# Kernel optimization log

Measured on AMD Instinct MI355X. Metric: run time of the kernel, lower is better.

Reference implementation:

```python
import jax, jax.numpy as jnp
import numpy as np

D_MODEL = 1024
N_HEAD = 16
DPH = D_MODEL // N_HEAD
NEG = -1e18


def setup_inputs() -> dict:
    key = jax.random.key(0)
    ks = jax.random.split(key, 8)
    B, L = 4, 2048
    k = jax.random.normal(ks[0], (B, L, D_MODEL), dtype=jnp.float32)
    v = jax.random.normal(ks[1], (B, L, D_MODEL), dtype=jnp.float32)
    q = jax.random.normal(ks[2], (B, L, D_MODEL), dtype=jnp.float32)
    attn_mask = jax.random.randint(ks[3], (B, L, L), 0, 2, dtype=jnp.int32)
    query_mask = jnp.ones((B, L), dtype=jnp.float32)
    # xavier_uniform bounds
    bnd1 = float(np.sqrt(6.0 / (3 * D_MODEL + D_MODEL)))
    bnd2 = float(np.sqrt(6.0 / (2 * D_MODEL)))
    kqv_w = jax.random.uniform(ks[4], (3 * D_MODEL, D_MODEL), minval=-bnd1, maxval=bnd1, dtype=jnp.float32)
    kqv_b = jnp.zeros((3 * D_MODEL,), dtype=jnp.float32)
    fin_w = jax.random.uniform(ks[5], (D_MODEL, D_MODEL), minval=-bnd2, maxval=bnd2, dtype=jnp.float32)
    fin_b = jnp.zeros((D_MODEL,), dtype=jnp.float32)
    return {"k": k, "v": v, "q": q, "attn_mask": attn_mask, "query_mask": query_mask,
            "kqv_w": kqv_w, "kqv_b": kqv_b, "fin_w": fin_w, "fin_b": fin_b}


def _split_heads(x, B):
    # [B, L, D] -> [B, H, L, dph]
    return x.reshape(B, -1, N_HEAD, DPH).transpose(0, 2, 1, 3)


def reference(k, v, q, attn_mask, query_mask, kqv_w, kqv_b, fin_w, fin_b):
    B = k.shape[0]
    scaling = DPH ** (-0.5)
    # three separate projections from one fused weight tensor (as in original)
    kp = k @ kqv_w[0:D_MODEL, :].T + kqv_b[0:D_MODEL]
    qp = q @ kqv_w[D_MODEL:2 * D_MODEL, :].T + kqv_b[D_MODEL:2 * D_MODEL]
    vp = v @ kqv_w[2 * D_MODEL:, :].T + kqv_b[2 * D_MODEL:]
    kh = _split_heads(kp, B)
    qh = _split_heads(qp, B) * scaling
    vh = _split_heads(vp, B)
    attn = jnp.einsum('bhqd,bhkd->bhqk', qh, kh)  # [B,H,Lq,Lk]
    if attn_mask is not None:
        attn = jnp.where(attn_mask[:, None, :, :] != 0, NEG, attn)
    attn = jax.nn.softmax(attn, axis=-1)
    # dropout: identity (eval mode / deterministic reference)
    context = jnp.einsum('bhqk,bhkd->bhqd', attn, vh)
    context = context.transpose(0, 2, 1, 3).reshape(B, -1, D_MODEL)
    context = context @ fin_w.T + fin_b
    attn_avg = attn.sum(axis=1) / N_HEAD  # [B,Lq,Lk]
    if query_mask is not None:
        qm = query_mask[:, :, None]
        context = context * qm
        attn_avg = attn_avg * qm
    return (context, attn_avg)
```

## Files before the change

kernel.cpp:

```cpp
#include <hip/hip_runtime.h>
#include <stdint.h>


typedef unsigned short u16;
typedef __attribute__((ext_vector_type(8))) short short8;
typedef __attribute__((ext_vector_type(4))) float f32x4;
typedef __attribute__((ext_vector_type(4))) float float4v;
typedef __attribute__((ext_vector_type(2))) unsigned int uint2v;

__device__ __forceinline__ u16 f2bf(float f){
  union { float f; uint32_t i; } c; c.f = f;
  return (u16)((c.i + 0x7FFFu + ((c.i >> 16) & 1u)) >> 16);
}
__device__ __forceinline__ short8 ld8(const u16* p){ return *(const short8*)p; }
__device__ __forceinline__ short8 ld8f(const float* p){
  const float4v a = *(const float4v*)p;
  const float4v b = *(const float4v*)(p + 4);
  short8 r;
  r[0] = (short)f2bf(a[0]); r[1] = (short)f2bf(a[1]);
  r[2] = (short)f2bf(a[2]); r[3] = (short)f2bf(a[3]);
  r[4] = (short)f2bf(b[0]); r[5] = (short)f2bf(b[1]);
  r[6] = (short)f2bf(b[2]); r[7] = (short)f2bf(b[3]);
  return r;
}
__device__ __forceinline__ float exp2_fast(float x){
  float r; asm("v_exp_f32 %0, %1" : "=v"(r) : "v"(x)); return r;
}
__device__ __forceinline__ uint32_t cvt_pk_bf16(float lo, float hi){
  uint32_t r;
  asm("v_cvt_pk_bf16_f32 %0, %1, %2" : "=v"(r) : "v"(lo), "v"(hi));
  return r;
}

#define MFMA(a,b,c) __builtin_amdgcn_mfma_f32_16x16x32_bf16((a),(b),(c),0,0,0)

__global__ void sentinel_k(float* out, float v){ out[0] = v; }

__global__ __launch_bounds__(256) void maskpack_k(const int* __restrict__ m,
                                                  uint64_t* __restrict__ bits){
  int t = blockIdx.x * 256 + threadIdx.x;
  uint64_t b = __ballot(m[t] != 0);
  if ((threadIdx.x & 63) == 0) bits[t >> 6] = b;
}

#define QLDA 40
__global__ __launch_bounds__(256) void qkv_gemm_k(
    const float* __restrict__ kin, const float* __restrict__ qin, const float* __restrict__ vin,
    const float* __restrict__ w, const float* __restrict__ bias,
    u16* __restrict__ qh, u16* __restrict__ kh, u16* __restrict__ vt)
{
  const int z = blockIdx.z;
  const float* A = (z == 0) ? kin : (z == 1) ? qin : vin;
  const float* W = w + (size_t)z * 1024 * 1024;
  const float* bs = bias + z * 1024;
  const int tileM = blockIdx.y * 64, tileN = blockIdx.x * 64;
  __shared__ __align__(16) u16 As[64 * QLDA];
  __shared__ __align__(16) u16 Bs[64 * QLDA];
  const int t = threadIdx.x, wave = t >> 6, lane = t & 63, quad = lane >> 4, mm = lane & 15;
  const int waveM = (wave >> 1) * 32, waveN = (wave & 1) * 32;
  f32x4 acc[2][2];
  for (int i = 0; i < 2; i++) for (int j = 0; j < 2; j++) acc[i][j] = (f32x4){0.f,0.f,0.f,0.f};
  const int lr = t >> 2, lc = (t & 3) * 8;
  for (int k0 = 0; k0 < 1024; k0 += 32){
    __syncthreads();
    *(short8*)&As[lr * QLDA + lc] = ld8f(&A[(size_t)(tileM + lr) * 1024 + k0 + lc]);
    *(short8*)&Bs[lr * QLDA + lc] = ld8f(&W[(size_t)(tileN + lr) * 1024 + k0 + lc]);
    __syncthreads();
    short8 a0 = *(const short8*)&As[(waveM + mm) * QLDA + quad * 8];
    short8 a1 = *(const short8*)&As[(waveM + 16 + mm) * QLDA + quad * 8];
    short8 b0 = *(const short8*)&Bs[(waveN + mm) * QLDA + quad * 8];
    short8 b1 = *(const short8*)&Bs[(waveN + 16 + mm) * QLDA + quad * 8];
    acc[0][0] = MFMA(a0, b0, acc[0][0]);
    acc[0][1] = MFMA(a0, b1, acc[0][1]);
    acc[1][0] = MFMA(a1, b0, acc[1][0]);
    acc[1][1] = MFMA(a1, b1, acc[1][1]);
  }
  const float scale = (z == 1) ? 0.18033688011112042f : 1.0f;
  for (int i = 0; i < 2; i++) for (int j = 0; j < 2; j++){
    int col = tileN + waveN + j * 16 + mm;
    float bv = bs[col];
    int h = col >> 6, d = col & 63;
    for (int r = 0; r < 4; r++){
      int row = tileM + waveM + i * 16 + quad * 4 + r;
      int bb = row >> 11, l = row & 2047;
      float v = (acc[i][j][r] + bv) * scale;
      if (z == 2)      vt[((bb * 16 + h) * 64 + d) * 2048 + l] = f2bf(v);
      else if (z == 1) qh[((bb * 16 + h) * 2048 + l) * 64 + d] = f2bf(v);
      else             kh[((bb * 16 + h) * 2048 + l) * 64 + d] = f2bf(v);
    }
  }
}

#define LDK 72
#define LDV 136
__global__ __launch_bounds__(256, 4) void flash_k(
    const u16* __restrict__ qh, const u16* __restrict__ kh, const u16* __restrict__ vt,
    const uint64_t* __restrict__ maskbits, u16* __restrict__ ctx,
    float* __restrict__ statsM, float* __restrict__ statsL)
{
  const int b = blockIdx.z, h = blockIdx.y, q0 = blockIdx.x * 64;
  const int t = threadIdx.x, wave = t >> 6, lane = t & 63, quad = lane >> 4, mm = lane & 15;
  __shared__ __align__(16) u16 Ks[128 * LDK];
  __shared__ __align__(16) u16 Vs[64 * LDV];
  const u16* qb = qh + (size_t)((b * 16 + h) * 2048) * 64;
  const u16* kb = kh + (size_t)((b * 16 + h) * 2048) * 64;
  const u16* vb = vt + (size_t)((b * 16 + h) * 64) * 2048;
  const int qrow = q0 + wave * 16 + mm;
  short8 qa0 = ld8(&qb[qrow * 64 + quad * 8]);
  short8 qa1 = ld8(&qb[qrow * 64 + 32 + quad * 8]);
  f32x4 O[4];
  for (int cb = 0; cb < 4; cb++) O[cb] = (f32x4){0.f,0.f,0.f,0.f};
  float mr = -30000.0f, lrn = 0.f;
  const uint64_t* mrow = maskbits + (size_t)(b * 2048 + qrow) * 32;

  for (int kt = 0; kt < 16; kt++){
    const int k0 = kt * 128;
    __syncthreads();
    #pragma unroll
    for (int i = 0; i < 4; i++){
      int ch = t + i * 256;
      int row = ch >> 3, c8 = (ch & 7) * 8;
      *(short8*)&Ks[row * LDK + c8] = ld8(&kb[(k0 + row) * 64 + c8]);
    }
    #pragma unroll
    for (int i = 0; i < 4; i++){
      int ch = t + i * 256;
      int row = ch >> 4, c8 = (ch & 15) * 8;
      *(short8*)&Vs[row * LDV + c8] = ld8(&vb[row * 2048 + k0 + c8]);
    }
    __syncthreads();
    f32x4 S[8];
    #pragma unroll
    for (int cb = 0; cb < 8; cb++){
      S[cb] = (f32x4){0.f,0.f,0.f,0.f};
      short8 kb0 = *(const short8*)&Ks[(cb * 16 + mm) * LDK + quad * 8];
      short8 kb1 = *(const short8*)&Ks[(cb * 16 + mm) * LDK + 32 + quad * 8];
      S[cb] = MFMA(kb0, qa0, S[cb]);
      S[cb] = MFMA(kb1, qa1, S[cb]);
    }
    uint64_t wq0 = mrow[2 * kt]     >> (quad * 4);
    uint64_t wq1 = mrow[2 * kt + 1] >> (quad * 4);
    #pragma unroll
    for (int cb = 0; cb < 8; cb++){
      uint32_t bits = (uint32_t)(((cb < 4) ? wq0 : wq1) >> (16 * (cb & 3)));
      #pragma unroll
      for (int r = 0; r < 4; r++)
        if (bits & (1u << r)) S[cb][r] = -1e30f;
    }
    f32x4 m4 = S[0];
    #pragma unroll
    for (int cb = 1; cb < 8; cb++)
      #pragma unroll
      for (int r = 0; r < 4; r++) m4[r] = fmaxf(m4[r], S[cb][r]);
    float tmax = fmaxf(fmaxf(m4[0], m4[1]), fmaxf(m4[2], m4[3]));
    tmax = fmaxf(tmax, __shfl_xor(tmax, 16, 64));
    tmax = fmaxf(tmax, __shfl_xor(tmax, 32, 64));
    float mnew  = fmaxf(mr, tmax);
    float alpha = exp2_fast(mr - mnew);
    f32x4 s4 = (f32x4){0.f,0.f,0.f,0.f};
    #pragma unroll
    for (int cb = 0; cb < 8; cb++)
      #pragma unroll
      for (int r = 0; r < 4; r++){
        float p = exp2_fast(S[cb][r] - mnew);
        S[cb][r] = p; s4[r] += p;
      }
    float tsum = (s4[0] + s4[1]) + (s4[2] + s4[3]);
    tsum += __shfl_xor(tsum, 16, 64);
    tsum += __shfl_xor(tsum, 32, 64);
    lrn = lrn * alpha + tsum;
    mr  = mnew;
    #pragma unroll
    for (int r = 0; r < 4; r++){
      float aq = __shfl(alpha, (lane & 48) | (quad * 4 + r), 64);
      #pragma unroll
      for (int cb = 0; cb < 4; cb++) O[cb][r] *= aq;
    }
    #pragma unroll
    for (int kc = 0; kc < 4; kc++){
      union { short8 s; uint32_t u[4]; } pa;
      pa.u[0] = cvt_pk_bf16(S[2 * kc][0],     S[2 * kc][1]);
      pa.u[1] = cvt_pk_bf16(S[2 * kc][2],     S[2 * kc][3]);
      pa.u[2] = cvt_pk_bf16(S[2 * kc + 1][0], S[2 * kc + 1][1]);
      pa.u[3] = cvt_pk_bf16(S[2 * kc + 1][2], S[2 * kc + 1][3]);
      #pragma unroll
      for (int cb = 0; cb < 4; cb++){
        union { short8 s; uint32_t u[4]; } vv;
        const uint2v vlo = *(const uint2v*)&Vs[(cb * 16 + mm) * LDV + kc * 32 + quad * 4];
        const uint2v vhi = *(const uint2v*)&Vs[(cb * 16 + mm) * LDV + kc * 32 + 16 + quad * 4];
        vv.u[0] = vlo[0]; vv.u[1] = vlo[1];
        vv.u[2] = vhi[0]; vv.u[3] = vhi[1];
        O[cb] = MFMA(pa.s, vv.s, O[cb]);
      }
    }
  }
  float inv = (lrn > 0.f) ? 1.0f / lrn : 0.f;
  #pragma unroll
  for (int r = 0; r < 4; r++){
    float invq = __shfl(inv, (lane & 48) | (quad * 4 + r), 64);
    int qg = q0 + wave * 16 + quad * 4 + r;
    #pragma unroll
    for (int cb = 0; cb < 4; cb++)
      ctx[(size_t)(b * 2048 + qg) * 1024 + h * 64 + cb * 16 + mm] = f2bf(O[cb][r] * invq);
  }
  if (quad == 0){
    statsM[(b * 16 + h) * 2048 + qrow] = mr;
    statsL[(b * 16 + h) * 2048 + qrow] = lrn;
  }
}

__global__ __launch_bounds__(256) void attnavg_k(
    const u16* __restrict__ qh, const u16* __restrict__ kh,
    const uint64_t* __restrict__ maskbits, const float* __restrict__ statsM,
    const float* __restrict__ statsL, const float* __restrict__ qmask,
    float* __restrict__ out2)
{
  const int b = blockIdx.z, q0 = blockIdx.y * 64, k0 = blockIdx.x * 64;
  const int t = threadIdx.x, wave = t >> 6, lane = t & 63, quad = lane >> 4, mm = lane & 15;
  __shared__ __align__(16) u16 Ks[64 * LDK];
  f32x4 acc[4];
  for (int cb = 0; cb < 4; cb++) acc[cb] = (f32x4){0.f,0.f,0.f,0.f};
  const int qg0 = q0 + wave * 16 + quad * 4;
  uint64_t wb[4];
  for (int r = 0; r < 4; r++)
    wb[r] = maskbits[(size_t)(b * 2048 + qg0 + r) * 32 + (k0 >> 6)];
  const int lr_ = t >> 2, lc_ = (t & 3) * 8;

  for (int h = 0; h < 16; h++){
    const u16* kb = kh + (size_t)((b * 16 + h) * 2048) * 64;
    const u16* qb = qh + (size_t)((b * 16 + h) * 2048) * 64;
    __syncthreads();
    *(short8*)&Ks[lr_ * LDK + lc_]      = ld8(&kb[(k0 + lr_) * 64 + lc_]);
    *(short8*)&Ks[lr_ * LDK + 32 + lc_] = ld8(&kb[(k0 + lr_) * 64 + 32 + lc_]);
    __syncthreads();
    const int qrow = q0 + wave * 16 + mm;
    short8 qa0 = ld8(&qb[qrow * 64 + quad * 8]);
    short8 qa1 = ld8(&qb[qrow * 64 + 32 + quad * 8]);
    f32x4 S[4];
    #pragma unroll
    for (int cb = 0; cb < 4; cb++){
      S[cb] = (f32x4){0.f,0.f,0.f,0.f};
      short8 kb0 = *(const short8*)&Ks[(cb * 16 + mm) * LDK + quad * 8];
      short8 kb1 = *(const short8*)&Ks[(cb * 16 + mm) * LDK + 32 + quad * 8];
      S[cb] = MFMA(qa0, kb0, S[cb]);
      S[cb] = MFMA(qa1, kb1, S[cb]);
    }
    #pragma unroll
    for (int r = 0; r < 4; r++){
      int sidx = (b * 16 + h) * 2048 + qg0 + r;
      float mh = statsM[sidx], lh = statsL[sidx];
      float sc = (lh > 0.f) ? 1.0f / (lh * 16.0f) : 0.f;
      #pragma unroll
      for (int cb = 0; cb < 4; cb++)
        if (!((wb[r] >> (cb * 16 + mm)) & 1ull))
          acc[cb][r] += exp2_fast(S[cb][r] - mh) * sc;
    }
  }
  for (int r = 0; r < 4; r++){
    int qg = qg0 + r;
    float qm = qmask[b * 2048 + qg];
    for (int cb = 0; cb < 4; cb++)
      out2[(size_t)(b * 2048 + qg) * 2048 + k0 + cb * 16 + mm] = acc[cb][r] * qm;
  }
}

__global__ __launch_bounds__(256) void fin_gemm_k(
    const u16* __restrict__ A, const float* __restrict__ W, const float* __restrict__ bias,
    const float* __restrict__ qmask, float* __restrict__ out)
{
  const int tileM = blockIdx.y * 64, tileN = blockIdx.x * 64;
  __shared__ __align__(16) u16 As[64 * QLDA];
  __shared__ __align__(16) u16 Bs[64 * QLDA];
  const int t = threadIdx.x, wave = t >> 6, lane = t & 63, quad = lane >> 4, mm = lane & 15;
  const int waveM = (wave >> 1) * 32, waveN = (wave & 1) * 32;
  f32x4 acc[2][2];
  for (int i = 0; i < 2; i++) for (int j = 0; j < 2; j++) acc[i][j] = (f32x4){0.f,0.f,0.f,0.f};
  const int lr = t >> 2, lc = (t & 3) * 8;
  for (int k0 = 0; k0 < 1024; k0 += 32){
    __syncthreads();
    *(short8*)&As[lr * QLDA + lc] = ld8(&A[(size_t)(tileM + lr) * 1024 + k0 + lc]);
    *(short8*)&Bs[lr * QLDA + lc] = ld8f(&W[(size_t)(tileN + lr) * 1024 + k0 + lc]);
    __syncthreads();
    short8 a0 = *(const short8*)&As[(waveM + mm) * QLDA + quad * 8];
    short8 a1 = *(const short8*)&As[(waveM + 16 + mm) * QLDA + quad * 8];
    short8 b0 = *(const short8*)&Bs[(waveN + mm) * QLDA + quad * 8];
    short8 b1 = *(const short8*)&Bs[(waveN + 16 + mm) * QLDA + quad * 8];
    acc[0][0] = MFMA(a0, b0, acc[0][0]);
    acc[0][1] = MFMA(a0, b1, acc[0][1]);
    acc[1][0] = MFMA(a1, b0, acc[1][0]);
    acc[1][1] = MFMA(a1, b1, acc[1][1]);
  }
  for (int i = 0; i < 2; i++) for (int j = 0; j < 2; j++){
    int col = tileN + waveN + j * 16 + mm;
    float bv = bias[col];
    for (int r = 0; r < 4; r++){
      int row = tileM + waveM + i * 16 + quad * 4 + r;
      float v = (acc[i][j][r] + bv) * qmask[row];
      out[(size_t)row * 1024 + col] = v;
    }
  }
}

extern "C" void kernel_launch(void* const* d_in, const int* in_sizes, int n_in,
                              void* d_out, int out_size, void* d_ws, size_t ws_size,
                              hipStream_t stream) {
  const float* k_in   = (const float*)d_in[0];
  const float* v_in   = (const float*)d_in[1];
  const float* q_in   = (const float*)d_in[2];
  const int*   amask  = (const int*)d_in[3];
  const float* qmask  = (const float*)d_in[4];
  const float* kqv_w  = (const float*)d_in[5];
  const float* kqv_b  = (const float*)d_in[6];
  const float* fin_w  = (const float*)d_in[7];
  const float* fin_b  = (const float*)d_in[8];
  float* out  = (float*)d_out;
  float* out2 = out + (size_t)8388608;

  const size_t WS_NEED = 36700160;
  if (ws_size < WS_NEED){
    sentinel_k<<<1, 1, 0, stream>>>(out, 1.0e6f + (float)(ws_size >> 20));
    return;
  }

  u16* qh  = (u16*)d_ws;
  u16* kh  = qh + (size_t)8388608;
  float* statsM = (float*)(kh + (size_t)8388608);
  float* statsL = statsM + 131072;
  uint64_t* maskbits = (uint64_t*)(statsL + 131072);
  u16* vt  = (u16*)out;
  u16* ctx = (u16*)out2;

  maskpack_k<<<dim3(65536), dim3(256), 0, stream>>>(amask, maskbits);
  qkv_gemm_k<<<dim3(16, 128, 3), dim3(256), 0, stream>>>(
      k_in, q_in, v_in, kqv_w, kqv_b, qh, kh, vt);
  flash_k<<<dim3(32, 16, 4), dim3(256), 0, stream>>>(
      qh, kh, vt, maskbits, ctx, statsM, statsL);
  fin_gemm_k<<<dim3(16, 128), dim3(256), 0, stream>>>(
      ctx, fin_w, fin_b, qmask, out);
  attnavg_k<<<dim3(32, 32, 4), dim3(256), 0, stream>>>(
      qh, kh, maskbits, statsM, statsL, qmask, out2);
}
```

Before: 771.4 us.

## Enlarge projection GEMM tiles to 128x128 and pack bf16 conversions and V stores

Both the QKV projection and the output projection GEMMs move from 64x64 to 128x128 block tiles, with each wave computing a 64x64 sub-tile of 4x4 MFMAs. This raises arithmetic intensity and cuts redundant global loads of the fp32 inputs and weights. The fp32-to-bf16 conversion now uses the packed hardware convert instruction, and the transposed V output is written as 4-element vector stores instead of scalar stores. The larger register footprint and the fourfold drop in block count may lower occupancy.

```diff
diff --git a/kernel.cpp b/kernel.cpp
--- a/kernel.cpp
+++ b/kernel.cpp
@@ -4,6 +4,7 @@
 
 typedef unsigned short u16;
 typedef __attribute__((ext_vector_type(8))) short short8;
+typedef __attribute__((ext_vector_type(4))) short short4v;
 typedef __attribute__((ext_vector_type(4))) float f32x4;
 typedef __attribute__((ext_vector_type(4))) float float4v;
 typedef __attribute__((ext_vector_type(2))) unsigned int uint2v;
@@ -13,23 +14,23 @@
   return (u16)((c.i + 0x7FFFu + ((c.i >> 16) & 1u)) >> 16);
 }
 __device__ __forceinline__ short8 ld8(const u16* p){ return *(const short8*)p; }
-__device__ __forceinline__ short8 ld8f(const float* p){
-  const float4v a = *(const float4v*)p;
-  const float4v b = *(const float4v*)(p + 4);
-  short8 r;
-  r[0] = (short)f2bf(a[0]); r[1] = (short)f2bf(a[1]);
-  r[2] = (short)f2bf(a[2]); r[3] = (short)f2bf(a[3]);
-  r[4] = (short)f2bf(b[0]); r[5] = (short)f2bf(b[1]);
-  r[6] = (short)f2bf(b[2]); r[7] = (short)f2bf(b[3]);
-  return r;
-}
-__device__ __forceinline__ float exp2_fast(float x){
-  float r; asm("v_exp_f32 %0, %1" : "=v"(r) : "v"(x)); return r;
-}
 __device__ __forceinline__ uint32_t cvt_pk_bf16(float lo, float hi){
   uint32_t r;
   asm("v_cvt_pk_bf16_f32 %0, %1, %2" : "=v"(r) : "v"(lo), "v"(hi));
   return r;
+}
+__device__ __forceinline__ short8 ld8f(const float* p){
+  const float4v a = *(const float4v*)p;
+  const float4v b = *(const float4v*)(p + 4);
+  union { short8 s; uint32_t u[4]; } r;
+  r.u[0] = cvt_pk_bf16(a[0], a[1]);
+  r.u[1] = cvt_pk_bf16(a[2], a[3]);
+  r.u[2] = cvt_pk_bf16(b[0], b[1]);
+  r.u[3] = cvt_pk_bf16(b[2], b[3]);
+  return r.s;
+}
+__device__ __forceinline__ float exp2_fast(float x){
+  float r; asm("v_exp_f32 %0, %1" : "=v"(r) : "v"(x)); return r;
 }
 
 #define MFMA(a,b,c) __builtin_amdgcn_mfma_f32_16x16x32_bf16((a),(b),(c),0,0,0)
@@ -53,42 +54,64 @@
   const float* A = (z == 0) ? kin : (z == 1) ? qin : vin;
   const float* W = w + (size_t)z * 1024 * 1024;
   const float* bs = bias + z * 1024;
-  const int tileM = blockIdx.y * 64, tileN = blockIdx.x * 64;
-  __shared__ __align__(16) u16 As[64 * QLDA];
-  __shared__ __align__(16) u16 Bs[64 * QLDA];
+  const int tileM = blockIdx.y * 128, tileN = blockIdx.x * 128;
+  __shared__ __align__(16) u16 As[128 * QLDA];
+  __shared__ __align__(16) u16 Bs[128 * QLDA];
   const int t = threadIdx.x, wave = t >> 6, lane = t & 63, quad = lane >> 4, mm = lane & 15;
-  const int waveM = (wave >> 1) * 32, waveN = (wave & 1) * 32;
-  f32x4 acc[2][2];
-  for (int i = 0; i < 2; i++) for (int j = 0; j < 2; j++) acc[i][j] = (f32x4){0.f,0.f,0.f,0.f};
-  const int lr = t >> 2, lc = (t & 3) * 8;
+  const int waveM = (wave >> 1) * 64, waveN = (wave & 1) * 64;
+  f32x4 acc[4][4];
+  #pragma unroll
+  for (int i = 0; i < 4; i++)
+    #pragma unroll
+    for (int j = 0; j < 4; j++) acc[i][j] = (f32x4){0.f,0.f,0.f,0.f};
+
   for (int k0 = 0; k0 < 1024; k0 += 32){
     __syncthreads();
-    *(short8*)&As[lr * QLDA + lc] = ld8f(&A[(size_t)(tileM + lr) * 1024 + k0 + lc]);
-    *(short8*)&Bs[lr * QLDA + lc] = ld8f(&W[(size_t)(tileN + lr) * 1024 + k0 + lc]);
-    __syncthreads();
-    short8 a0 = *(const short8*)&As[(waveM + mm) * QLDA + quad * 8];
-    short8 a1 = *(const short8*)&As[(waveM + 16 + mm) * QLDA + quad * 8];
-    short8 b0 = *(const short8*)&Bs[(waveN + mm) * QLDA + quad * 8];
-    short8 b1 = *(const short8*)&Bs[(waveN + 16 + mm) * QLDA + quad * 8];
-    acc[0][0] = MFMA(a0, b0, acc[0][0]);
-    acc[0][1] = MFMA(a0, b1, acc[0][1]);
-    acc[1][0] = MFMA(a1, b0, acc[1][0]);
-    acc[1][1] = MFMA(a1, b1, acc[1][1]);
+    #pragma unroll
+    for (int i = 0; i < 2; i++){
+      int ch = t + i * 256;
+      int row = ch >> 2, lc = (ch & 3) * 8;
+      *(short8*)&As[row * QLDA + lc] = ld8f(&A[(size_t)(tileM + row) * 1024 + k0 + lc]);
+      *(short8*)&Bs[row * QLDA + lc] = ld8f(&W[(size_t)(tileN + row) * 1024 + k0 + lc]);
+    }
+    __syncthreads();
+    short8 af[4], bf[4];
+    #pragma unroll
+    for (int m = 0; m < 4; m++) af[m] = *(const short8*)&As[(waveM + m * 16 + mm) * QLDA + quad * 8];
+    #pragma unroll
+    for (int n = 0; n < 4; n++) bf[n] = *(const short8*)&Bs[(waveN + n * 16 + mm) * QLDA + quad * 8];
+    #pragma unroll
+    for (int m = 0; m < 4; m++)
+      #pragma unroll
+      for (int n = 0; n < 4; n++)
+        acc[m][n] = MFMA(af[m], bf[n], acc[m][n]);
   }
   const float scale = (z == 1) ? 0.18033688011112042f : 1.0f;
-  for (int i = 0; i < 2; i++) for (int j = 0; j < 2; j++){
-    int col = tileN + waveN + j * 16 + mm;
-    float bv = bs[col];
-    int h = col >> 6, d = col & 63;
-    for (int r = 0; r < 4; r++){
-      int row = tileM + waveM + i * 16 + quad * 4 + r;
-      int bb = row >> 11, l = row & 2047;
-      float v = (acc[i][j][r] + bv) * scale;
-      if (z == 2)      vt[((bb * 16 + h) * 64 + d) * 2048 + l] = f2bf(v);
-      else if (z == 1) qh[((bb * 16 + h) * 2048 + l) * 64 + d] = f2bf(v);
-      else             kh[((bb * 16 + h) * 2048 + l) * 64 + d] = f2bf(v);
-    }
-  }
+  #pragma unroll
+  for (int m = 0; m < 4; m++)
+    #pragma unroll
+    for (int n = 0; n < 4; n++){
+      int col = tileN + waveN + n * 16 + mm;
+      float bv = bs[col];
+      int h = col >> 6, d = col & 63;
+      int row0 = tileM + waveM + m * 16 + quad * 4;
+      if (z == 2){
+        int bb = row0 >> 11, l0 = row0 & 2047;
+        union { short4v s; uint32_t u[2]; } pk;
+        pk.u[0] = cvt_pk_bf16(acc[m][n][0] + bv, acc[m][n][1] + bv);
+        pk.u[1] = cvt_pk_bf16(acc[m][n][2] + bv, acc[m][n][3] + bv);
+        *(short4v*)&vt[((size_t)(bb * 16 + h) * 64 + d) * 2048 + l0] = pk.s;
+      } else {
+        u16* dst = (z == 1) ? qh : kh;
+        #pragma unroll
+        for (int r = 0; r < 4; r++){
+          int row = row0 + r;
+          int bb = row >> 11, l = row & 2047;
+          float v = (acc[m][n][r] + bv) * scale;
+          dst[((size_t)(bb * 16 + h) * 2048 + l) * 64 + d] = f2bf(v);
+        }
+      }
+    }
 }
 
 #define LDK 72
@@ -268,37 +291,51 @@
     const u16* __restrict__ A, const float* __restrict__ W, const float* __restrict__ bias,
     const float* __restrict__ qmask, float* __restrict__ out)
 {
-  const int tileM = blockIdx.y * 64, tileN = blockIdx.x * 64;
-  __shared__ __align__(16) u16 As[64 * QLDA];
-  __shared__ __align__(16) u16 Bs[64 * QLDA];
+  const int tileM = blockIdx.y * 128, tileN = blockIdx.x * 128;
+  __shared__ __align__(16) u16 As[128 * QLDA];
+  __shared__ __align__(16) u16 Bs[128 * QLDA];
   const int t = threadIdx.x, wave = t >> 6, lane = t & 63, quad = lane >> 4, mm = lane & 15;
-  const int waveM = (wave >> 1) * 32, waveN = (wave & 1) * 32;
-  f32x4 acc[2][2];
-  for (int i = 0; i < 2; i++) for (int j = 0; j < 2; j++) acc[i][j] = (f32x4){0.f,0.f,0.f,0.f};
-  const int lr = t >> 2, lc = (t & 3) * 8;
+  const int waveM = (wave >> 1) * 64, waveN = (wave & 1) * 64;
+  f32x4 acc[4][4];
+  #pragma unroll
+  for (int i = 0; i < 4; i++)
+    #pragma unroll
+    for (int j = 0; j < 4; j++) acc[i][j] = (f32x4){0.f,0.f,0.f,0.f};
+
   for (int k0 = 0; k0 < 1024; k0 += 32){
     __syncthreads();
-    *(short8*)&As[lr * QLDA + lc] = ld8(&A[(size_t)(tileM + lr) * 1024 + k0 + lc]);
-    *(short8*)&Bs[lr * QLDA + lc] = ld8f(&W[(size_t)(tileN + lr) * 1024 + k0 + lc]);
-    __syncthreads();
-    short8 a0 = *(const short8*)&As[(waveM + mm) * QLDA + quad * 8];
-    short8 a1 = *(const short8*)&As[(waveM + 16 + mm) * QLDA + quad * 8];
-    short8 b0 = *(const short8*)&Bs[(waveN + mm) * QLDA + quad * 8];
-    short8 b1 = *(const short8*)&Bs[(waveN + 16 + mm) * QLDA + quad * 8];
-    acc[0][0] = MFMA(a0, b0, acc[0][0]);
-    acc[0][1] = MFMA(a0, b1, acc[0][1]);
-    acc[1][0] = MFMA(a1, b0, acc[1][0]);
-    acc[1][1] = MFMA(a1, b1, acc[1][1]);
-  }
-  for (int i = 0; i < 2; i++) for (int j = 0; j < 2; j++){
-    int col = tileN + waveN + j * 16 + mm;
-    float bv = bias[col];
-    for (int r = 0; r < 4; r++){
-      int row = tileM + waveM + i * 16 + quad * 4 + r;
-      float v = (acc[i][j][r] + bv) * qmask[row];
-      out[(size_t)row * 1024 + col] = v;
-    }
-  }
+    #pragma unroll
+    for (int i = 0; i < 2; i++){
+      int ch = t + i * 256;
+      int row = ch >> 2, lc = (ch & 3) * 8;
+      *(short8*)&As[row * QLDA + lc] = ld8(&A[(size_t)(tileM + row) * 1024 + k0 + lc]);
+      *(short8*)&Bs[row * QLDA + lc] = ld8f(&W[(size_t)(tileN + row) * 1024 + k0 + lc]);
+    }
+    __syncthreads();
+    short8 af[4], bf[4];
+    #pragma unroll
+    for (int m = 0; m < 4; m++) af[m] = *(const short8*)&As[(waveM + m * 16 + mm) * QLDA + quad * 8];
+    #pragma unroll
+    for (int n = 0; n < 4; n++) bf[n] = *(const short8*)&Bs[(waveN + n * 16 + mm) * QLDA + quad * 8];
+    #pragma unroll
+    for (int m = 0; m < 4; m++)
+      #pragma unroll
+      for (int n = 0; n < 4; n++)
+        acc[m][n] = MFMA(af[m], bf[n], acc[m][n]);
+  }
+  #pragma unroll
+  for (int m = 0; m < 4; m++)
+    #pragma unroll
+    for (int n = 0; n < 4; n++){
+      int col = tileN + waveN + n * 16 + mm;
+      float bv = bias[col];
+      #pragma unroll
+      for (int r = 0; r < 4; r++){
+        int row = tileM + waveM + m * 16 + quad * 4 + r;
+        float v = (acc[m][n][r] + bv) * qmask[row];
+        out[(size_t)row * 1024 + col] = v;
+      }
+    }
 }
 
 extern "C" void kernel_launch(void* const* d_in, const int* in_sizes, int n_in,
@@ -331,11 +368,11 @@
   u16* ctx = (u16*)out2;
 
   maskpack_k<<<dim3(65536), dim3(256), 0, stream>>>(amask, maskbits);
-  qkv_gemm_k<<<dim3(16, 128, 3), dim3(256), 0, stream>>>(
+  qkv_gemm_k<<<dim3(8, 64, 3), dim3(256), 0, stream>>>(
       k_in, q_in, v_in, kqv_w, kqv_b, qh, kh, vt);
   flash_k<<<dim3(32, 16, 4), dim3(256), 0, stream>>>(
       qh, kh, vt, maskbits, ctx, statsM, statsL);
-  fin_gemm_k<<<dim3(16, 128), dim3(256), 0, stream>>>(
+  fin_gemm_k<<<dim3(8, 64), dim3(256), 0, stream>>>(
       ctx, fin_w, fin_b, qmask, out);
   attnavg_k<<<dim3(32, 32, 4), dim3(256), 0, stream>>>(
       qh, kh, maskbits, statsM, statsL, qmask, out2);
```

Measured after the change: 711.7 us. 1.08x faster.
